# Optimization experiments

Hardware: AMD Instinct MI355X
Metric: run time of the kernel (lower is better)

The kernel has to match this reference:

```python
import jax, jax.numpy as jnp
import numpy as np
from math import sqrt

B, L, S, H, E = 4, 2048, 2048, 8, 64
T = 1.0  # softmax temperature


def setup_inputs() -> dict:
    key = jax.random.key(0)
    kq, kk, kv = jax.random.split(key, 3)
    q = jax.random.normal(kq, (B, L, H, E), dtype=jnp.float32)
    k = jax.random.normal(kk, (B, S, H, E), dtype=jnp.float32)
    v = jax.random.normal(kv, (B, S, H, E), dtype=jnp.float32)
    mask = jnp.zeros((B, L), dtype=jnp.bool_)  # unused by the module, kept for signature fidelity
    return {"q": q, "k": k, "v": v, "mask": mask}


def reference(q, k, v, mask):
    Bq, Lq, Hq, Eq = q.shape
    # [B,L,H,E] -> [B,H,E,L]; FFT over time axis
    xq = jnp.transpose(q, (0, 2, 3, 1))
    xk = jnp.transpose(k, (0, 2, 3, 1))
    xv = jnpp_t = jnp.transpose(v, (0, 2, 3, 1))
    xq_ft = jnp.fft.rfft(xq, axis=-1, norm='ortho')   # [B,H,E,Lf]
    xk_ft = jnp.fft.rfft(xk, axis=-1, norm='ortho')   # [B,H,E,Sf]
    xv_ft = jnp.fft.rfft(xv, axis=-1, norm='ortho')   # [B,H,E,Sf]
    # complex frequency-domain scores [B,H,Lf,Sf]
    scores = jnp.einsum('bhex,bhey->bhxy', xq_ft, jnp.conj(xk_ft)) / sqrt(Eq)
    # activation == 'softmax': softmax over |scores|/T, then real-weighted complex mix
    attn = jax.nn.softmax(jnp.abs(scores) / T, axis=-1)
    xqkv_ft = jnp.einsum('bhxy,bhey->bhex', attn.astype(xv_ft.dtype), xv_ft)  # [B,H,E,Lf]
    out = jnp.fft.irfft(xqkv_ft, n=Lq, axis=-1, norm='ortho')  # [B,H,E,L]
    return jnp.transpose(out, (0, 3, 1, 2))  # [B,L,H,E]
```

## Files before the change

kernel.cpp:

```cpp
#include <hip/hip_runtime.h>
#include <hip/hip_bf16.h>
#include <math.h>

#define LOGN  11
#define NN    2048
#define LOGM  10
#define MM    1024
#define NF    1025
#define NYP   1056
#define TWO_PI 6.283185307179586f
#define INV_SQRT_N 0.022097086912079608f
#define INV_SCALE  0.044194173824159216f
#define LOG2E      1.4426950408889634f

typedef __attribute__((ext_vector_type(8))) short bhalf8;
typedef __attribute__((ext_vector_type(4))) float f32x4;

#define MFMA16(a, b, c) __builtin_amdgcn_mfma_f32_16x16x32_bf16(a, b, c, 0, 0, 0)

#define GLD16(gp, lp)                                                              \
    __builtin_amdgcn_global_load_lds(                                              \
        (const __attribute__((address_space(1))) void*)(gp),                       \
        (__attribute__((address_space(3))) void*)(lp), 16, 0, 0)

#define CVTPK(dst, lo, hi) \
    asm("v_cvt_pk_bf16_f32 %0, %1, %2" : "=v"(dst) : "v"(lo), "v"(hi))

#define EXP2F(dst, src) \
    asm("v_exp_f32 %0, %1" : "=v"(dst) : "v"(src))

__device__ __forceinline__ unsigned short f2bf(float f) {
    union { float f; unsigned u; } v; v.f = f;
    unsigned r = v.u + 0x7FFFu + ((v.u >> 16) & 1u);
    return (unsigned short)(r >> 16);
}
__device__ __forceinline__ float bf2f(unsigned short h) {
    union { unsigned u; float f; } v; v.u = ((unsigned)h) << 16;
    return v.f;
}

__device__ __forceinline__ int dr4_10(unsigned j) {
    unsigned r = __brev(j) >> 22;
    return (int)(((r & 0x155u) << 1) | ((r >> 1) & 0x155u));
}

template<bool FWD>
__device__ __forceinline__ void fft_r4_1024(float2* buf, const float2* tw, int tid)
{
    {
        int i0 = tid * 4;
        float2 a = buf[i0], b = buf[i0 + 1], c = buf[i0 + 2], d = buf[i0 + 3];
        float2 apc = make_float2(a.x + c.x, a.y + c.y);
        float2 amc = make_float2(a.x - c.x, a.y - c.y);
        float2 bpd = make_float2(b.x + d.x, b.y + d.y);
        float2 bmd = make_float2(b.x - d.x, b.y - d.y);
        buf[i0]     = make_float2(apc.x + bpd.x, apc.y + bpd.y);
        buf[i0 + 2] = make_float2(apc.x - bpd.x, apc.y - bpd.y);
        if (FWD) {
            buf[i0 + 1] = make_float2(amc.x + bmd.y, amc.y - bmd.x);
            buf[i0 + 3] = make_float2(amc.x - bmd.y, amc.y + bmd.x);
        } else {
            buf[i0 + 1] = make_float2(amc.x - bmd.y, amc.y + bmd.x);
            buf[i0 + 3] = make_float2(amc.x + bmd.y, amc.y - bmd.x);
        }
        __syncthreads();
    }
    #pragma unroll
    for (int s = 1; s < 5; s++) {
        int L  = 1 << (2 * s);
        int p  = tid & (L - 1);
        int i0 = ((tid >> (2 * s)) << (2 * s + 2)) + p;
        int e  = p << (8 - 2 * s);
        float2 w1 = tw[e], w2 = tw[2 * e], w3 = tw[3 * e];
        float2 a  = buf[i0];
        float2 xb = buf[i0 + L], xc = buf[i0 + 2 * L], xd = buf[i0 + 3 * L];
        float2 b = make_float2(xb.x * w1.x - xb.y * w1.y, xb.x * w1.y + xb.y * w1.x);
        float2 c = make_float2(xc.x * w2.x - xc.y * w2.y, xc.x * w2.y + xc.y * w2.x);
        float2 d = make_float2(xd.x * w3.x - xd.y * w3.y, xd.x * w3.y + xd.y * w3.x);
        float2 apc = make_float2(a.x + c.x, a.y + c.y);
        float2 amc = make_float2(a.x - c.x, a.y - c.y);
        float2 bpd = make_float2(b.x + d.x, b.y + d.y);
        float2 bmd = make_float2(b.x - d.x, b.y - d.y);
        buf[i0]         = make_float2(apc.x + bpd.x, apc.y + bpd.y);
        buf[i0 + 2 * L] = make_float2(apc.x - bpd.x, apc.y - bpd.y);
        if (FWD) {
            buf[i0 + L]     = make_float2(amc.x + bmd.y, amc.y - bmd.x);
            buf[i0 + 3 * L] = make_float2(amc.x - bmd.y, amc.y + bmd.x);
        } else {
            buf[i0 + L]     = make_float2(amc.x - bmd.y, amc.y + bmd.x);
            buf[i0 + 3 * L] = make_float2(amc.x + bmd.y, amc.y - bmd.x);
        }
        __syncthreads();
    }
}

__global__ __launch_bounds__(256) void tr_fwd(const float* __restrict__ q,
                                              const float* __restrict__ k,
                                              const float* __restrict__ v,
                                              unsigned short* __restrict__ ttr)
{
    __shared__ float Ts[64][65];
    int tt     = blockIdx.x;
    int h      = blockIdx.y;
    int z      = blockIdx.z;
    int tensor = z >> 2;
    int b      = z & 3;
    int tid    = threadIdx.x;
    int t0     = tt * 64;

    const float* in = (tensor == 0) ? q : (tensor == 1) ? k : v;

    {
        int tl = tid >> 2, ec = (tid & 3) * 16;
        const float* src = in + ((size_t)b * 2048 + t0 + tl) * 512 + h * 64 + ec;
        #pragma unroll
        for (int m = 0; m < 4; m++) {
            float4 v4 = *(const float4*)(src + m * 4);
            Ts[tl][ec + m * 4 + 0] = v4.x;
            Ts[tl][ec + m * 4 + 1] = v4.y;
            Ts[tl][ec + m * 4 + 2] = v4.z;
            Ts[tl][ec + m * 4 + 3] = v4.w;
        }
    }
    __syncthreads();
    {
        int el = tid >> 2, tc = (tid & 3) * 16;
        size_t row = ((size_t)(tensor * 32 + b * 8 + h)) * 64 + el;
        unsigned short* dst = ttr + row * 2048 + t0 + tc;
        #pragma unroll
        for (int m = 0; m < 4; m++) {
            float a0 = Ts[tc + m * 4 + 0][el], a1 = Ts[tc + m * 4 + 1][el];
            float a2 = Ts[tc + m * 4 + 2][el], a3 = Ts[tc + m * 4 + 3][el];
            unsigned u0, u1;
            CVTPK(u0, a0, a1);
            CVTPK(u1, a2, a3);
            uint2 o; o.x = u0; o.y = u1;
            *(uint2*)(dst + m * 4) = o;
        }
    }
}

__global__ __launch_bounds__(256) void fft_fwd(const unsigned short* __restrict__ ttr,
                                               unsigned short* __restrict__ Pq,
                                               unsigned short* __restrict__ Pk,
                                               unsigned short* __restrict__ Pv)
{
    __shared__ float2 buf[MM];
    __shared__ float2 tw[768];

    int g      = blockIdx.x;
    int p      = g % 96;
    int e      = g / 96;
    int tensor = p / 32;
    int bh     = p % 32;
    int tid    = threadIdx.x;

    unsigned short* plane = (tensor == 0) ? Pq : (tensor == 1) ? Pk : Pv;
    float scl = (tensor == 0) ? (INV_SQRT_N * 0.125f * LOG2E) : INV_SQRT_N;
    int vk3 = (tensor == 2) ? (((e >> 2) & 3) << 3) : 0;

    #pragma unroll
    for (int i = tid; i < 768; i += 256) {
        float ang = -TWO_PI * (float)i / (float)MM;
        float sv, cv;
        __sincosf(ang, &sv, &cv);
        tw[i] = make_float2(cv, sv);
    }

    const unsigned short* src = ttr + ((size_t)p * 64 + e) * 2048;
    #pragma unroll
    for (int i = 0; i < 4; i++) {
        int j = tid + 256 * i;
        unsigned pr = *(const unsigned*)(src + 2 * j);
        float x0 = bf2f((unsigned short)(pr & 0xFFFFu));
        float x1 = bf2f((unsigned short)(pr >> 16));
        buf[dr4_10((unsigned)j)] = make_float2(x0, x1);
    }
    __syncthreads();

    fft_r4_1024<true>(buf, tw, tid);

    unsigned short* dre = plane + ((size_t)bh * 128 + e) * NYP;
    unsigned short* dim_ = dre + (size_t)64 * NYP;

#define RPOINT(Ai, Bi, KKi, XR, XI) do {                                   \
        float Ex = 0.5f * (Ai.x + Bi.x), Ey = 0.5f * (Ai.y - Bi.y);        \
        float Dx = 0.5f * (Ai.x - Bi.x), Dy = 0.5f * (Ai.y + Bi.y);        \
        float Ox = Dy, Oy = -Dx;                                           \
        float th = -(TWO_PI / (float)NN) * (float)(KKi);                   \
        float sn, cs; __sincosf(th, &sn, &cs);                             \
        XR = (Ex + cs * Ox - sn * Oy) * scl;                               \
        XI = (Ey + cs * Oy + sn * Ox) * scl;                               \
    } while (0)

    #pragma unroll
    for (int i = 0; i < 2; i++) {
        int kk = 2 * tid + 512 * i;
        float2 A0 = buf[kk];
        float2 B0 = buf[(MM - kk) & (MM - 1)];
        float2 A1 = buf[kk + 1];
        float2 B1 = buf[MM - kk - 1];
        float Xr0, Xi0, Xr1, Xi1;
        RPOINT(A0, B0, kk, Xr0, Xi0);
        RPOINT(A1, B1, kk + 1, Xr1, Xi1);
        unsigned ur, ui;
        CVTPK(ur, Xr0, Xr1);
        CVTPK(ui, Xi0, Xi1);
        int ks = kk ^ vk3;
        *(unsigned*)(dre + ks)  = ur;
        *(unsigned*)(dim_ + ks) = ui;
    }
    if (tid < 16) {
        unsigned ur = 0, ui = 0;
        if (tid == 0) {
            float2 A = buf[0];
            float sn, cs;
            __sincosf(-(TWO_PI / (float)NN) * 1024.0f, &sn, &cs);
            float Xr = (A.x + cs * A.y) * scl;
            float Xi = (sn * A.y) * scl;
            float zz = 0.f;
            CVTPK(ur, Xr, zz);
            CVTPK(ui, Xi, zz);
        }
        int ks = (1024 + 2 * tid) ^ vk3;
        *(unsigned*)(dre + ks)  = ur;
        *(unsigned*)(dim_ + ks) = ui;
    }
#undef RPOINT
}

__global__ __launch_bounds__(256) void qkpack(const unsigned short* __restrict__ Pq,
                                              const unsigned short* __restrict__ Pk,
                                              unsigned short* __restrict__ Qp,
                                              unsigned short* __restrict__ Kp)
{
    __shared__ unsigned short Ts[32][136];
    int y0  = blockIdx.x * 32;
    int bh  = blockIdx.y;
    int tsr = blockIdx.z;
    int tid = threadIdx.x;

    const unsigned short* srcp = (tsr == 0) ? Pq : Pk;
    unsigned short* dstp       = (tsr == 0) ? Qp : Kp;

    {
        int kk = tid >> 1, seg = tid & 1;
        const unsigned short* sp = srcp + ((size_t)bh * 128 + kk) * NYP + y0 + seg * 16;
        uint4 va = *(const uint4*)sp;
        uint4 vb = *(const uint4*)(sp + 8);
        const unsigned short* pa = (const unsigned short*)&va;
        const unsigned short* pb = (const unsigned short*)&vb;
        #pragma unroll
        for (int j = 0; j < 8; j++) Ts[seg * 16 + j][kk] = pa[j];
        #pragma unroll
        for (int j = 0; j < 8; j++) Ts[seg * 16 + 8 + j][kk] = pb[j];
    }
    __syncthreads();
    {
        int y = tid >> 3, c = tid & 7;
        uint4 lo = *(const uint4*)&Ts[y][c * 16];
        uint4 hi = *(const uint4*)&Ts[y][c * 16 + 8];
        char* rowb = (char*)(dstp + ((size_t)bh * NYP + y0 + y) * 128);
        if (tsr == 0) {
            *(uint4*)(rowb + c * 32)      = lo;
            *(uint4*)(rowb + c * 32 + 16) = hi;
        } else {
            int s = y & 7;
            *(uint4*)(rowb + (((2 * c)     ^ s) << 4)) = lo;
            *(uint4*)(rowb + (((2 * c + 1) ^ s) << 4)) = hi;
        }
    }
}

struct FlashShared {
    union {
        struct {
            unsigned short Ks[2][32][128];
            unsigned short Vs[2][128][32];
        } kv;
        unsigned short OutT[128][72];
    } u;
    unsigned short Ps[4][16][40];
};

template<int NH>
__global__ __launch_bounds__(256) void flash_mfma(
    const unsigned short* __restrict__ Qp,
    const unsigned short* __restrict__ Kp,
    const unsigned short* __restrict__ Vt,
    unsigned short* __restrict__ nb0,
    unsigned short* __restrict__ nb1,
    float* __restrict__ lbuf)
{
    __shared__ FlashShared S;

    int g    = blockIdx.x;
    int bh   = g & 31;
    int idx  = g >> 5;
    int half = idx / 17;
    int x0   = (idx % 17) * 64;
    int tid  = threadIdx.x;
    int w    = tid >> 6;
    int lane = tid & 63;
    int qd   = lane >> 4;
    int col  = lane & 15;

    int xrow = x0 + w * 16 + col;
    int xq   = min(xrow, 1024);
    const unsigned short* qb = Qp + ((size_t)bh * NYP + xq) * 128 + qd * 8;
    bhalf8 Are[4], Aim[4];
    #pragma unroll
    for (int ks = 0; ks < 4; ks++) Are[ks] = *(const bhalf8*)(qb + ks * 32);
    Aim[0] = Are[2];
    Aim[1] = Are[3];
    #pragma unroll
    for (int ks = 0; ks < 2; ks++) {
        bhalf8 t = Are[ks];
        unsigned* u = (unsigned*)&t;
        #pragma unroll
        for (int j = 0; j < 4; j++) u[j] ^= 0x80008000u;
        Aim[ks + 2] = t;
    }

    f32x4 O[8];
    #pragma unroll
    for (int n = 0; n < 8; n++) O[n] = (f32x4){0.f, 0.f, 0.f, 0.f};
    float Lacc[4] = {0.f, 0.f, 0.f, 0.f};

    int yt0 = (half * 33) / NH, yt1 = ((half + 1) * 33) / NH;

    const char* ksrc = (const char*)Kp
        + ((size_t)bh * NYP + (size_t)yt0 * 32 + w * 8) * 256 + lane * 16;
    const char* vbase = (const char*)Vt + (size_t)bh * 128 * (NYP * 2);
    const char* vsrc0 = vbase + ((size_t)(w * 32) + (lane >> 2)) * (NYP * 2)
                        + (size_t)yt0 * 64 + (lane & 3) * 16;
    const char* vsrc1 = vsrc0 + (size_t)16 * (NYP * 2);

    int sw = col & 7;
    int kco[4];
    #pragma unroll
    for (int ks = 0; ks < 4; ks++) kco[ks] = ((ks * 4 + qd) ^ sw) * 8;
    int vq = (qd ^ ((col >> 2) & 3)) * 8;

    {
        int pb = yt0 & 1;
        GLD16(ksrc,         &S.u.kv.Ks[pb][w * 8][0]);
        GLD16(ksrc + 1024,  &S.u.kv.Ks[pb][w * 8 + 4][0]);
        GLD16(vsrc0,        &S.u.kv.Vs[pb][w * 32][0]);
        GLD16(vsrc1,        &S.u.kv.Vs[pb][w * 32 + 16][0]);
        ksrc += 8192; vsrc0 += 64; vsrc1 += 64;
    }

    for (int yt = yt0; yt < yt1; yt++) {
        int cb = yt & 1, nb = cb ^ 1;
        if (yt + 1 < yt1) {
            GLD16(ksrc,         &S.u.kv.Ks[nb][w * 8][0]);
            GLD16(ksrc + 1024,  &S.u.kv.Ks[nb][w * 8 + 4][0]);
            GLD16(vsrc0,        &S.u.kv.Vs[nb][w * 32][0]);
            GLD16(vsrc1,        &S.u.kv.Vs[nb][w * 32 + 16][0]);
            ksrc += 8192; vsrc0 += 64; vsrc1 += 64;
            __builtin_amdgcn_sched_barrier(0);
            asm volatile("s_waitcnt vmcnt(4)" ::: "memory");
        } else {
            __builtin_amdgcn_sched_barrier(0);
            asm volatile("s_waitcnt vmcnt(0)" ::: "memory");
        }
        __builtin_amdgcn_sched_barrier(0);
        __builtin_amdgcn_s_barrier();
        __builtin_amdgcn_sched_barrier(0);

        const unsigned short* k0 = &S.u.kv.Ks[cb][col][0];
        const unsigned short* k1 = &S.u.kv.Ks[cb][col + 16][0];

        f32x4 sre[2], sim[2];
        #pragma unroll
        for (int sc = 0; sc < 2; sc++) {
            sre[sc] = (f32x4){0.f, 0.f, 0.f, 0.f};
            sim[sc] = (f32x4){0.f, 0.f, 0.f, 0.f};
        }
        __builtin_amdgcn_s_setprio(1);
        #pragma unroll
        for (int ks = 0; ks < 4; ks++) {
            bhalf8 b0 = *(const bhalf8*)(k0 + kco[ks]);
            bhalf8 b1 = *(const bhalf8*)(k1 + kco[ks]);
            sre[0] = MFMA16(Are[ks], b0, sre[0]);
            sim[0] = MFMA16(Aim[ks], b0, sim[0]);
            sre[1] = MFMA16(Are[ks], b1, sre[1]);
            sim[1] = MFMA16(Aim[ks], b1, sim[1]);
        }
        __builtin_amdgcn_s_setprio(0);

        #pragma unroll
        for (int r = 0; r < 4; r++) {
            float re0 = sre[0][r], im0 = sim[0][r];
            float re1 = sre[1][r], im1 = sim[1][r];
            float s0 = __builtin_amdgcn_sqrtf(fmaf(re0, re0, im0 * im0));
            float s1 = __builtin_amdgcn_sqrtf(fmaf(re1, re1, im1 * im1));
            float p0, p1;
            EXP2F(p0, s0);
            EXP2F(p1, s1);
            Lacc[r] += p0 + p1;
            unsigned up;
            CVTPK(up, p0, p1);
            S.Ps[w][qd * 4 + r][col]      = (unsigned short)up;
            S.Ps[w][qd * 4 + r][col + 16] = (unsigned short)(up >> 16);
        }

        bhalf8 pa = *(const bhalf8*)&S.Ps[w][col][qd * 8];
        __builtin_amdgcn_s_setprio(1);
        #pragma unroll
        for (int n = 0; n < 8; n++) {
            bhalf8 bv = *(const bhalf8*)&S.u.kv.Vs[cb][n * 16 + col][vq];
            O[n] = MFMA16(pa, bv, O[n]);
        }
        __builtin_amdgcn_s_setprio(0);

        asm volatile("s_waitcnt lgkmcnt(0)" ::: "memory");
        __builtin_amdgcn_sched_barrier(0);
        __builtin_amdgcn_s_barrier();
        __builtin_amdgcn_sched_barrier(0);
    }

    #pragma unroll
    for (int r = 0; r < 4; r++) {
        float ls = Lacc[r];
        ls += __shfl_xor(ls, 1);
        ls += __shfl_xor(ls, 2);
        ls += __shfl_xor(ls, 4);
        ls += __shfl_xor(ls, 8);
        if (yt1 == 33) ls -= 31.0f;
        int x = x0 + w * 16 + qd * 4 + r;
        if (x <= 1024 && col == 0)
            lbuf[((size_t)half * 32 + bh) * NYP + x] = ls;
    }

    const size_t HSZ = (size_t)32 * 128 * NYP;
    unsigned short* nplane = (half < 2 ? nb0 : nb1) + (size_t)(half & 1) * HSZ;

    __syncthreads();
    #pragma unroll
    for (int n = 0; n < 8; n++) {
        unsigned u0, u1;
        CVTPK(u0, O[n][0], O[n][1]);
        CVTPK(u1, O[n][2], O[n][3]);
        *(unsigned*)&S.u.OutT[n * 16 + col][w * 16 + qd * 4]     = u0;
        *(unsigned*)&S.u.OutT[n * 16 + col][w * 16 + qd * 4 + 2] = u1;
    }
    __syncthreads();
    {
        int kk2 = tid >> 1, seg = tid & 1;
        int xg  = x0 + seg * 32;
        if (xg < NYP) {
            unsigned short* dst = nplane + ((size_t)bh * 128 + kk2) * NYP + xg;
            const unsigned short* srcl = &S.u.OutT[kk2][seg * 32];
            #pragma unroll
            for (int m = 0; m < 4; m++)
                *(uint4*)(dst + m * 8) = *(const uint4*)(srcl + m * 8);
        }
    }
}

template<int NH>
__global__ __launch_bounds__(256) void fft_inv(const unsigned short* __restrict__ nb0,
                                               const unsigned short* __restrict__ nb1,
                                               const float* __restrict__ lbuf,
                                               float* __restrict__ st)
{
    __shared__ float2 buf[MM];
    __shared__ float2 tw[768];

    int s   = blockIdx.x;
    int e   = s & 63;
    int bh  = s >> 6;
    int tid = threadIdx.x;

    #pragma unroll
    for (int i = tid; i < 768; i += 256) {
        float ang = TWO_PI * (float)i / (float)MM;
        float sv, cv;
        __sincosf(ang, &sv, &cv);
        tw[i] = make_float2(cv, sv);
    }

    const size_t HSZ = (size_t)32 * 128 * NYP;
    const unsigned short* pre[NH];
    const unsigned short* pim[NH];
    const float* lb[NH];
    #pragma unroll
    for (int h = 0; h < NH; h++) {
        const unsigned short* base = (h < 2 ? nb0 : nb1) + (size_t)(h & 1) * HSZ;
        pre[h] = base + ((size_t)bh * 128 + e) * NYP;
        pim[h] = base + ((size_t)bh * 128 + 64 + e) * NYP;
        lb[h]  = lbuf + ((size_t)h * 32 + bh) * NYP;
    }

    #pragma unroll
    for (int i = 0; i < 4; i++) {
        int kk = tid + 256 * i;
        int x1 = kk, x2 = 1024 - kk;
        float d1 = 0.f, d2 = 0.f;
        float Axs = 0.f, Ays = 0.f, Bxs = 0.f, Bys = 0.f;
        #pragma unroll
        for (int h = 0; h < NH; h++) {
            d1 += lb[h][x1];
            d2 += lb[h][x2];
            Axs += bf2f(pre[h][x1]);
            Ays += bf2f(pim[h][x1]);
            Bxs += bf2f(pre[h][x2]);
            Bys += bf2f(pim[h][x2]);
        }
        float iv1 = 1.f / d1, iv2 = 1.f / d2;
        float Ax = Axs * iv1, Ay = Ays * iv1;
        float Bx = Bxs * iv2, By = -(Bys * iv2);
        float Ex = 0.5f * (Ax + Bx), Ey = 0.5f * (Ay + By);
        float Dx = 0.5f * (Ax - Bx), Dy = 0.5f * (Ay - By);
        float th = (TWO_PI / (float)NN) * (float)kk;
        float sn, cs;
        __sincosf(th, &sn, &cs);
        float Ox = Dx * cs - Dy * sn;
        float Oy = Dx * sn + Dy * cs;
        buf[dr4_10((unsigned)kk)] = make_float2(Ex - Oy, Ey + Ox);
    }
    __syncthreads();

    fft_r4_1024<false>(buf, tw, tid);

    float* dst = st + ((size_t)bh * 64 + e) * 2048;
    #pragma unroll
    for (int i = 0; i < 4; i++) {
        int j = tid + 256 * i;
        float2 z = buf[j];
        *(float2*)&dst[2 * j] = make_float2(z.x * INV_SCALE, z.y * INV_SCALE);
    }
}

__global__ __launch_bounds__(256) void out_tr(const float* __restrict__ st,
                                              float* __restrict__ out)
{
    __shared__ float Ts[64][65];
    int tt  = blockIdx.x;
    int h   = blockIdx.y;
    int b   = blockIdx.z;
    int tid = threadIdx.x;
    int bh  = b * 8 + h;

    {
        int e = tid >> 2, tc = (tid & 3) * 16;
        const float* src = st + ((size_t)bh * 64 + e) * 2048 + tt * 64 + tc;
        #pragma unroll
        for (int m = 0; m < 4; m++) {
            float4 v4 = *(const float4*)(src + m * 4);
            Ts[e][tc + m * 4 + 0] = v4.x;
            Ts[e][tc + m * 4 + 1] = v4.y;
            Ts[e][tc + m * 4 + 2] = v4.z;
            Ts[e][tc + m * 4 + 3] = v4.w;
        }
    }
    __syncthreads();
    {
        int t = tid >> 2, ec = (tid & 3) * 16;
        float* dst = out + (size_t)b * 2048 * 512 + (size_t)(tt * 64 + t) * 512
                     + h * 64 + ec;
        #pragma unroll
        for (int m = 0; m < 4; m++) {
            float4 v4;
            v4.x = Ts[ec + m * 4 + 0][t];
            v4.y = Ts[ec + m * 4 + 1][t];
            v4.z = Ts[ec + m * 4 + 2][t];
            v4.w = Ts[ec + m * 4 + 3][t];
            *(float4*)(dst + m * 4) = v4;
        }
    }
}

extern "C" void kernel_launch(void* const* d_in, const int* in_sizes, int n_in,
                              void* d_out, int out_size, void* d_ws, size_t ws_size,
                              hipStream_t stream)
{
    const float* q = (const float*)d_in[0];
    const float* k = (const float*)d_in[1];
    const float* v = (const float*)d_in[2];
    float* out = (float*)d_out;

    char* ws = (char*)d_ws;
    const size_t PL = (size_t)32 * 128 * NYP * sizeof(unsigned short);
    unsigned short* Pq = (unsigned short*)(ws);
    unsigned short* Pk = (unsigned short*)(ws + PL);
    unsigned short* Pv = (unsigned short*)(ws + 2 * PL);
    unsigned short* ttr = (unsigned short*)(ws + 3 * PL);
    unsigned short* Qp = (unsigned short*)(ws + 3 * PL);
    unsigned short* Kp = (unsigned short*)(ws + 4 * PL);
    float* st = (float*)(ws + 3 * PL);

    const size_t lbuf4 = (size_t)4 * 32 * NYP * sizeof(float);
    bool big = ws_size >= 7 * PL + lbuf4;

    hipLaunchKernelGGL(tr_fwd, dim3(32, 8, 12), dim3(256), 0, stream,
                       q, k, v, ttr);
    hipLaunchKernelGGL(fft_fwd, dim3(3 * 2048), dim3(256), 0, stream,
                       ttr, Pq, Pk, Pv);
    hipLaunchKernelGGL(qkpack, dim3(33, 32, 2), dim3(256), 0, stream,
                       Pq, Pk, Qp, Kp);

    if (big) {
        unsigned short* nb0 = (unsigned short*)(ws);
        unsigned short* nb1 = (unsigned short*)(ws + 5 * PL);
        float* lbuf = (float*)(ws + 7 * PL);
        hipLaunchKernelGGL((flash_mfma<4>), dim3(17 * 4 * 32), dim3(256), 0, stream,
                           Qp, Kp, Pv, nb0, nb1, lbuf);
        hipLaunchKernelGGL((fft_inv<4>), dim3(2048), dim3(256), 0, stream,
                           nb0, nb1, lbuf, st);
    } else {
        unsigned short* nb0 = (unsigned short*)(ws);
        float* lbuf = (float*)(ws + 5 * PL);
        hipLaunchKernelGGL((flash_mfma<2>), dim3(17 * 2 * 32), dim3(256), 0, stream,
                           Qp, Kp, Pv, nb0, nb0, lbuf);
        hipLaunchKernelGGL((fft_inv<2>), dim3(2048), dim3(256), 0, stream,
                           nb0, nb0, lbuf, st);
    }

    hipLaunchKernelGGL(out_tr, dim3(32, 8, 4), dim3(256), 0, stream,
                       st, out);
}
```

Measured before the change: 207.3 us.

## Precompute FFT twiddle tables once and pad LDS FFT buffers against bank conflicts

Adds a small kernel that builds forward/inverse radix-4 twiddles and the real-FFT post-processing cos/sin table once per call. The forward and inverse FFT kernels then load these from global memory instead of evaluating sincos per block and per point. The LDS FFT buffers are also padded by one element every 16 to cut bank conflicts in strided butterfly accesses. This adds one extra launch and small global table reads, and slightly enlarges LDS use per block.

```diff
diff --git a/kernel.cpp b/kernel.cpp
--- a/kernel.cpp
+++ b/kernel.cpp
@@ -13,6 +13,10 @@
 #define INV_SCALE  0.044194173824159216f
 #define LOG2E      1.4426950408889634f
 
+#define PAD(i) ((i) + ((i) >> 4))
+#define MMP   1088
+#define TWP   816
+
 typedef __attribute__((ext_vector_type(8))) short bhalf8;
 typedef __attribute__((ext_vector_type(4))) float f32x4;
 
@@ -44,24 +48,45 @@
     return (int)(((r & 0x155u) << 1) | ((r >> 1) & 0x155u));
 }
 
+__global__ __launch_bounds__(256) void mk_tables(float2* __restrict__ twf,
+                                                 float2* __restrict__ twi,
+                                                 float2* __restrict__ rc)
+{
+    int i = blockIdx.x * 256 + threadIdx.x;
+    if (i < 768) {
+        float ang = TWO_PI * (float)i / (float)MM;
+        float sv, cv;
+        __sincosf(ang, &sv, &cv);
+        twf[i] = make_float2(cv, -sv);
+        twi[i] = make_float2(cv,  sv);
+    }
+    if (i < 1025) {
+        float ang = TWO_PI * (float)i / (float)NN;
+        float sv, cv;
+        __sincosf(ang, &sv, &cv);
+        rc[i] = make_float2(cv, sv);
+    }
+}
+
 template<bool FWD>
 __device__ __forceinline__ void fft_r4_1024(float2* buf, const float2* tw, int tid)
 {
     {
         int i0 = tid * 4;
-        float2 a = buf[i0], b = buf[i0 + 1], c = buf[i0 + 2], d = buf[i0 + 3];
+        int q0 = PAD(i0), q1 = PAD(i0 + 1), q2 = PAD(i0 + 2), q3 = PAD(i0 + 3);
+        float2 a = buf[q0], b = buf[q1], c = buf[q2], d = buf[q3];
         float2 apc = make_float2(a.x + c.x, a.y + c.y);
         float2 amc = make_float2(a.x - c.x, a.y - c.y);
         float2 bpd = make_float2(b.x + d.x, b.y + d.y);
         float2 bmd = make_float2(b.x - d.x, b.y - d.y);
-        buf[i0]     = make_float2(apc.x + bpd.x, apc.y + bpd.y);
-        buf[i0 + 2] = make_float2(apc.x - bpd.x, apc.y - bpd.y);
+        buf[q0] = make_float2(apc.x + bpd.x, apc.y + bpd.y);
+        buf[q2] = make_float2(apc.x - bpd.x, apc.y - bpd.y);
         if (FWD) {
-            buf[i0 + 1] = make_float2(amc.x + bmd.y, amc.y - bmd.x);
-            buf[i0 + 3] = make_float2(amc.x - bmd.y, amc.y + bmd.x);
+            buf[q1] = make_float2(amc.x + bmd.y, amc.y - bmd.x);
+            buf[q3] = make_float2(amc.x - bmd.y, amc.y + bmd.x);
         } else {
-            buf[i0 + 1] = make_float2(amc.x - bmd.y, amc.y + bmd.x);
-            buf[i0 + 3] = make_float2(amc.x + bmd.y, amc.y - bmd.x);
+            buf[q1] = make_float2(amc.x - bmd.y, amc.y + bmd.x);
+            buf[q3] = make_float2(amc.x + bmd.y, amc.y - bmd.x);
         }
         __syncthreads();
     }
@@ -71,9 +96,10 @@
         int p  = tid & (L - 1);
         int i0 = ((tid >> (2 * s)) << (2 * s + 2)) + p;
         int e  = p << (8 - 2 * s);
-        float2 w1 = tw[e], w2 = tw[2 * e], w3 = tw[3 * e];
-        float2 a  = buf[i0];
-        float2 xb = buf[i0 + L], xc = buf[i0 + 2 * L], xd = buf[i0 + 3 * L];
+        float2 w1 = tw[PAD(e)], w2 = tw[PAD(2 * e)], w3 = tw[PAD(3 * e)];
+        int q0 = PAD(i0), q1 = PAD(i0 + L), q2 = PAD(i0 + 2 * L), q3 = PAD(i0 + 3 * L);
+        float2 a  = buf[q0];
+        float2 xb = buf[q1], xc = buf[q2], xd = buf[q3];
         float2 b = make_float2(xb.x * w1.x - xb.y * w1.y, xb.x * w1.y + xb.y * w1.x);
         float2 c = make_float2(xc.x * w2.x - xc.y * w2.y, xc.x * w2.y + xc.y * w2.x);
         float2 d = make_float2(xd.x * w3.x - xd.y * w3.y, xd.x * w3.y + xd.y * w3.x);
@@ -81,14 +107,14 @@
         float2 amc = make_float2(a.x - c.x, a.y - c.y);
         float2 bpd = make_float2(b.x + d.x, b.y + d.y);
         float2 bmd = make_float2(b.x - d.x, b.y - d.y);
-        buf[i0]         = make_float2(apc.x + bpd.x, apc.y + bpd.y);
-        buf[i0 + 2 * L] = make_float2(apc.x - bpd.x, apc.y - bpd.y);
+        buf[q0] = make_float2(apc.x + bpd.x, apc.y + bpd.y);
+        buf[q2] = make_float2(apc.x - bpd.x, apc.y - bpd.y);
         if (FWD) {
-            buf[i0 + L]     = make_float2(amc.x + bmd.y, amc.y - bmd.x);
-            buf[i0 + 3 * L] = make_float2(amc.x - bmd.y, amc.y + bmd.x);
+            buf[q1] = make_float2(amc.x + bmd.y, amc.y - bmd.x);
+            buf[q3] = make_float2(amc.x - bmd.y, amc.y + bmd.x);
         } else {
-            buf[i0 + L]     = make_float2(amc.x - bmd.y, amc.y + bmd.x);
-            buf[i0 + 3 * L] = make_float2(amc.x + bmd.y, amc.y - bmd.x);
+            buf[q1] = make_float2(amc.x - bmd.y, amc.y + bmd.x);
+            buf[q3] = make_float2(amc.x + bmd.y, amc.y - bmd.x);
         }
         __syncthreads();
     }
@@ -141,12 +167,14 @@
 }
 
 __global__ __launch_bounds__(256) void fft_fwd(const unsigned short* __restrict__ ttr,
+                                               const float2* __restrict__ twg,
+                                               const float2* __restrict__ rc,
                                                unsigned short* __restrict__ Pq,
                                                unsigned short* __restrict__ Pk,
                                                unsigned short* __restrict__ Pv)
 {
-    __shared__ float2 buf[MM];
-    __shared__ float2 tw[768];
+    __shared__ float2 buf[MMP];
+    __shared__ float2 tw[TWP];
 
     int g      = blockIdx.x;
     int p      = g % 96;
@@ -160,12 +188,7 @@
     int vk3 = (tensor == 2) ? (((e >> 2) & 3) << 3) : 0;
 
     #pragma unroll
-    for (int i = tid; i < 768; i += 256) {
-        float ang = -TWO_PI * (float)i / (float)MM;
-        float sv, cv;
-        __sincosf(ang, &sv, &cv);
-        tw[i] = make_float2(cv, sv);
-    }
+    for (int i = tid; i < 768; i += 256) tw[PAD(i)] = twg[i];
 
     const unsigned short* src = ttr + ((size_t)p * 64 + e) * 2048;
     #pragma unroll
@@ -174,7 +197,7 @@
         unsigned pr = *(const unsigned*)(src + 2 * j);
         float x0 = bf2f((unsigned short)(pr & 0xFFFFu));
         float x1 = bf2f((unsigned short)(pr >> 16));
-        buf[dr4_10((unsigned)j)] = make_float2(x0, x1);
+        buf[PAD(dr4_10((unsigned)j))] = make_float2(x0, x1);
     }
     __syncthreads();
 
@@ -183,26 +206,25 @@
     unsigned short* dre = plane + ((size_t)bh * 128 + e) * NYP;
     unsigned short* dim_ = dre + (size_t)64 * NYP;
 
-#define RPOINT(Ai, Bi, KKi, XR, XI) do {                                   \
+#define RPOINT(Ai, Bi, CX, CY, XR, XI) do {                                \
         float Ex = 0.5f * (Ai.x + Bi.x), Ey = 0.5f * (Ai.y - Bi.y);        \
         float Dx = 0.5f * (Ai.x - Bi.x), Dy = 0.5f * (Ai.y + Bi.y);        \
         float Ox = Dy, Oy = -Dx;                                           \
-        float th = -(TWO_PI / (float)NN) * (float)(KKi);                   \
-        float sn, cs; __sincosf(th, &sn, &cs);                             \
-        XR = (Ex + cs * Ox - sn * Oy) * scl;                               \
-        XI = (Ey + cs * Oy + sn * Ox) * scl;                               \
+        XR = (Ex + (CX) * Ox + (CY) * Oy) * scl;                           \
+        XI = (Ey + (CX) * Oy - (CY) * Ox) * scl;                           \
     } while (0)
 
     #pragma unroll
     for (int i = 0; i < 2; i++) {
         int kk = 2 * tid + 512 * i;
-        float2 A0 = buf[kk];
-        float2 B0 = buf[(MM - kk) & (MM - 1)];
-        float2 A1 = buf[kk + 1];
-        float2 B1 = buf[MM - kk - 1];
+        float2 A0 = buf[PAD(kk)];
+        float2 B0 = buf[PAD((MM - kk) & (MM - 1))];
+        float2 A1 = buf[PAD(kk + 1)];
+        float2 B1 = buf[PAD(MM - kk - 1)];
+        float4 rq = *(const float4*)(&rc[kk]);
         float Xr0, Xi0, Xr1, Xi1;
-        RPOINT(A0, B0, kk, Xr0, Xi0);
-        RPOINT(A1, B1, kk + 1, Xr1, Xi1);
+        RPOINT(A0, B0, rq.x, rq.y, Xr0, Xi0);
+        RPOINT(A1, B1, rq.z, rq.w, Xr1, Xi1);
         unsigned ur, ui;
         CVTPK(ur, Xr0, Xr1);
         CVTPK(ui, Xi0, Xi1);
@@ -213,14 +235,10 @@
     if (tid < 16) {
         unsigned ur = 0, ui = 0;
         if (tid == 0) {
-            float2 A = buf[0];
-            float sn, cs;
-            __sincosf(-(TWO_PI / (float)NN) * 1024.0f, &sn, &cs);
-            float Xr = (A.x + cs * A.y) * scl;
-            float Xi = (sn * A.y) * scl;
+            float2 A = buf[PAD(0)];
+            float Xr = (A.x - A.y) * scl;
             float zz = 0.f;
             CVTPK(ur, Xr, zz);
-            CVTPK(ui, Xi, zz);
         }
         int ks = (1024 + 2 * tid) ^ vk3;
         *(unsigned*)(dre + ks)  = ur;
@@ -463,11 +481,13 @@
 template<int NH>
 __global__ __launch_bounds__(256) void fft_inv(const unsigned short* __restrict__ nb0,
                                                const unsigned short* __restrict__ nb1,
+                                               const float2* __restrict__ twg,
+                                               const float2* __restrict__ rc,
                                                const float* __restrict__ lbuf,
                                                float* __restrict__ st)
 {
-    __shared__ float2 buf[MM];
-    __shared__ float2 tw[768];
+    __shared__ float2 buf[MMP];
+    __shared__ float2 tw[TWP];
 
     int s   = blockIdx.x;
     int e   = s & 63;
@@ -475,12 +495,7 @@
     int tid = threadIdx.x;
 
     #pragma unroll
-    for (int i = tid; i < 768; i += 256) {
-        float ang = TWO_PI * (float)i / (float)MM;
-        float sv, cv;
-        __sincosf(ang, &sv, &cv);
-        tw[i] = make_float2(cv, sv);
-    }
+    for (int i = tid; i < 768; i += 256) tw[PAD(i)] = twg[i];
 
     const size_t HSZ = (size_t)32 * 128 * NYP;
     const unsigned short* pre[NH];
@@ -514,12 +529,10 @@
         float Bx = Bxs * iv2, By = -(Bys * iv2);
         float Ex = 0.5f * (Ax + Bx), Ey = 0.5f * (Ay + By);
         float Dx = 0.5f * (Ax - Bx), Dy = 0.5f * (Ay - By);
-        float th = (TWO_PI / (float)NN) * (float)kk;
-        float sn, cs;
-        __sincosf(th, &sn, &cs);
-        float Ox = Dx * cs - Dy * sn;
-        float Oy = Dx * sn + Dy * cs;
-        buf[dr4_10((unsigned)kk)] = make_float2(Ex - Oy, Ey + Ox);
+        float2 rcv = rc[kk];
+        float Ox = Dx * rcv.x - Dy * rcv.y;
+        float Oy = Dx * rcv.y + Dy * rcv.x;
+        buf[PAD(dr4_10((unsigned)kk))] = make_float2(Ex - Oy, Ey + Ox);
     }
     __syncthreads();
 
@@ -529,7 +542,7 @@
     #pragma unroll
     for (int i = 0; i < 4; i++) {
         int j = tid + 256 * i;
-        float2 z = buf[j];
+        float2 z = buf[PAD(j)];
         *(float2*)&dst[2 * j] = make_float2(z.x * INV_SCALE, z.y * INV_SCALE);
     }
 }
@@ -593,12 +606,20 @@
     float* st = (float*)(ws + 3 * PL);
 
     const size_t lbuf4 = (size_t)4 * 32 * NYP * sizeof(float);
-    bool big = ws_size >= 7 * PL + lbuf4;
-
+    const size_t lbuf2 = (size_t)2 * 32 * NYP * sizeof(float);
+    const size_t TBL   = (size_t)(768 + 768 + 1025) * sizeof(float2);
+    bool big = ws_size >= 7 * PL + lbuf4 + TBL;
+
+    char* tb = big ? (ws + 7 * PL + lbuf4) : (ws + 5 * PL + lbuf2);
+    float2* twf = (float2*)tb;
+    float2* twi = twf + 768;
+    float2* rc  = twi + 768;
+
+    hipLaunchKernelGGL(mk_tables, dim3(5), dim3(256), 0, stream, twf, twi, rc);
     hipLaunchKernelGGL(tr_fwd, dim3(32, 8, 12), dim3(256), 0, stream,
                        q, k, v, ttr);
     hipLaunchKernelGGL(fft_fwd, dim3(3 * 2048), dim3(256), 0, stream,
-                       ttr, Pq, Pk, Pv);
+                       ttr, twf, rc, Pq, Pk, Pv);
     hipLaunchKernelGGL(qkpack, dim3(33, 32, 2), dim3(256), 0, stream,
                        Pq, Pk, Qp, Kp);
 
@@ -609,14 +630,14 @@
         hipLaunchKernelGGL((flash_mfma<4>), dim3(17 * 4 * 32), dim3(256), 0, stream,
                            Qp, Kp, Pv, nb0, nb1, lbuf);
         hipLaunchKernelGGL((fft_inv<4>), dim3(2048), dim3(256), 0, stream,
-                           nb0, nb1, lbuf, st);
+                           nb0, nb1, twi, rc, lbuf, st);
     } else {
         unsigned short* nb0 = (unsigned short*)(ws);
         float* lbuf = (float*)(ws + 5 * PL);
         hipLaunchKernelGGL((flash_mfma<2>), dim3(17 * 2 * 32), dim3(256), 0, stream,
                            Qp, Kp, Pv, nb0, nb0, lbuf);
         hipLaunchKernelGGL((fft_inv<2>), dim3(2048), dim3(256), 0, stream,
-                           nb0, nb0, lbuf, st);
+                           nb0, nb0, twi, rc, lbuf, st);
     }
 
     hipLaunchKernelGGL(out_tr, dim3(32, 8, 4), dim3(256), 0, stream,
```

After: 197.7 us. 4.6% less time.
